# Kernel tuning notes

Hardware: AMD Instinct MI355X
Metric: run time of the kernel (lower is better)

The kernel has to match this reference:

```python
import jax, jax.numpy as jnp
import numpy as np

N_NODES = 100000
N_EDGES = 1600000
DIM = 32
BN_EPS = 1e-5


def setup_inputs() -> dict:
    key = jax.random.key(0)
    ks = jax.random.split(key, 5)
    h = jax.random.normal(ks[0], (N_NODES, DIM), dtype=jnp.float32)
    e = jax.random.normal(ks[1], (N_EDGES, DIM), dtype=jnp.float32)
    norm = jax.random.uniform(ks[2], (N_NODES, 1), dtype=jnp.float32)
    src = jax.random.randint(ks[3], (N_EDGES,), 0, N_NODES, dtype=jnp.int32)
    dst = jax.random.randint(ks[4], (N_EDGES,), 0, N_NODES, dtype=jnp.int32)
    return {
        "h": h, "e": e, "norm": norm, "src": src, "dst": dst,
        "gamma_h": jnp.ones((DIM,), jnp.float32),
        "beta_h": jnp.zeros((DIM,), jnp.float32),
        "gamma_e": jnp.ones((DIM,), jnp.float32),
        "beta_e": jnp.zeros((DIM,), jnp.float32),
    }


def _batch_norm(x, gamma, beta):
    # training-mode BatchNorm1d: biased batch statistics over axis 0
    mean = jnp.mean(x, axis=0)
    var = jnp.var(x, axis=0)
    return (x - mean) * jax.lax.rsqrt(var + BN_EPS) * gamma + beta


def reference(h, e, norm, src, dst, gamma_h, beta_h, gamma_e, beta_e):
    n_nodes = h.shape[0]
    h = h * norm                                  # [N, d]
    # per-edge gate: e_ij = Ce + Dh_src + Eh_dst (all identity projections)
    e_ij = e + h[src] + h[dst]                    # [E, d]
    sigma = jax.nn.sigmoid(e_ij)                  # [E, d]
    # gated weighted-mean aggregation onto destination nodes
    num = jax.ops.segment_sum(sigma * h[src], dst, num_segments=n_nodes)
    den = jax.ops.segment_sum(sigma, dst, num_segments=n_nodes)
    h_new = h + num / (den + 1e-6)                # zero-indegree nodes: h + 0
    h_new = h_new * norm
    # batch norm (training mode), then activation; dropout is identity in eval
    h_out = jax.nn.relu(_batch_norm(h_new, gamma_h, beta_h))
    e_out = jax.nn.relu(_batch_norm(e_ij, gamma_e, beta_e))
    return h_out, e_out
```

## Files before the change

### kernel.cpp

```cpp
#include <hip/hip_runtime.h>

#define NN 100000
#define NE 1600000
#define DIMS 32
static constexpr int SCOPIES = 32;

typedef float fx4 __attribute__((ext_vector_type(4)));

#define NBUCK 1024
#define NPB   98
#define B1    128
#define CHUNK (NE / B1)

static constexpr long long OFF_HNB   = 0;
static constexpr long long OFF_SE    = 1600000;
static constexpr long long OFF_SH    = 1602048;
static constexpr long long OFF_FIN   = 1604096;
static constexpr long long OFF_OFFS  = 1604224;
static constexpr long long OFF_BBASE = 1704226;
static constexpr long long OFF_HIST  = 1705252;
static constexpr long long OFF_REC   = 1836324;
static constexpr long long OFF_EID2  = 5036324;

__device__ __forceinline__ ushort bf16rn(float f) {
  unsigned u = __float_as_uint(f);
  unsigned r = (u + 0x7FFFu + ((u >> 16) & 1u)) >> 16;
  return (ushort)r;
}
__device__ __forceinline__ float bf16tof(ushort s) {
  return __uint_as_float(((unsigned)s) << 16);
}

__global__ __launch_bounds__(256) void k_hn(const float* __restrict__ h,
                                            const float* __restrict__ norm,
                                            ushort* __restrict__ hnb) {
  int i = blockIdx.x * blockDim.x + threadIdx.x;
  if (i >= NN * 8) return;
  float4 v = reinterpret_cast<const float4*>(h)[i];
  float nm = norm[i >> 3];
  ushort4 o;
  o.x = bf16rn(v.x * nm);
  o.y = bf16rn(v.y * nm);
  o.z = bf16rn(v.z * nm);
  o.w = bf16rn(v.w * nm);
  reinterpret_cast<ushort4*>(hnb)[i] = o;
}

__global__ __launch_bounds__(256) void k_bh(const int* __restrict__ dst,
                                            int* __restrict__ hist) {
  __shared__ int cnt[NBUCK];
  const int t = threadIdx.x, b = blockIdx.x;
  for (int j = t; j < NBUCK; j += 256) cnt[j] = 0;
  __syncthreads();
  const int lo = b * CHUNK, hi = lo + CHUNK;
  for (int i = lo + t; i < hi; i += 256) atomicAdd(&cnt[dst[i] / NPB], 1);
  __syncthreads();
  for (int j = t; j < NBUCK; j += 256) hist[j * B1 + b] = cnt[j];
}

__global__ __launch_bounds__(1024) void k_bscan(int* __restrict__ hist,
                                                int* __restrict__ bbase) {
  __shared__ int sh[NBUCK];
  const int t = threadIdx.x;
  int tot = 0;
  for (int i = 0; i < B1; ++i) tot += hist[t * B1 + i];
  sh[t] = tot;
  __syncthreads();
  for (int d = 1; d < NBUCK; d <<= 1) {
    int v = (t >= d) ? sh[t - d] : 0;
    __syncthreads();
    sh[t] += v;
    __syncthreads();
  }
  int excl = sh[t] - tot;
  bbase[t] = excl;
  if (t == NBUCK - 1) bbase[NBUCK] = NE;
  int run = excl;
  for (int i = 0; i < B1; ++i) {
    int c = hist[t * B1 + i];
    hist[t * B1 + i] = run;
    run += c;
  }
}

__global__ __launch_bounds__(256) void k_bscat(const int* __restrict__ src,
                                               const int* __restrict__ dst,
                                               const int* __restrict__ hist,
                                               unsigned long long* __restrict__ rec) {
  __shared__ int cur[NBUCK];
  const int t = threadIdx.x, b = blockIdx.x;
  for (int j = t; j < NBUCK; j += 256) cur[j] = hist[j * B1 + b];
  __syncthreads();
  const int lo = b * CHUNK, hi = lo + CHUNK;
  for (int i = lo + t; i < hi; i += 256) {
    int d = dst[i], s = src[i];
    int bk = d / NPB;
    int pos = atomicAdd(&cur[bk], 1);
    rec[pos] = (unsigned long long)i |
               ((unsigned long long)s << 21) |
               ((unsigned long long)d << 38);
  }
}

__global__ __launch_bounds__(256) void k_bsort(const unsigned long long* __restrict__ rec,
                                               const int* __restrict__ bbase,
                                               int2* __restrict__ eid2,
                                               int* __restrict__ offs) {
  __shared__ int cnt[NPB];
  __shared__ int curq[NPB];
  __shared__ int2 sorted[2048];
  const int t = threadIdx.x, b = blockIdx.x;
  const int base_e = bbase[b];
  const int n = bbase[b + 1] - base_e;
  const int nodebase = b * NPB;
  if (t < NPB) cnt[t] = 0;
  __syncthreads();
  for (int i = t; i < n; i += 256) {
    int d = (int)((rec[base_e + i] >> 38) & 0x1FFFF);
    atomicAdd(&cnt[d - nodebase], 1);
  }
  __syncthreads();
  if (t == 0) {
    int run = 0;
    for (int j = 0; j < NPB; ++j) {
      int c = cnt[j];
      cnt[j] = run;
      curq[j] = run;
      run += c;
    }
  }
  __syncthreads();
  for (int i = t; i < n; i += 256) {
    unsigned long long r = rec[base_e + i];
    int k = (int)(r & 0x1FFFFF);
    int s = (int)((r >> 21) & 0x1FFFF);
    int d = (int)((r >> 38) & 0x1FFFF);
    int pos = atomicAdd(&curq[d - nodebase], 1);
    if (pos < 2048) sorted[pos] = make_int2(k, s);
  }
  __syncthreads();
  for (int i = t; i < n; i += 256) eid2[base_e + i] = sorted[i];
  for (int j = t; j < NPB; j += 256) {
    int node = nodebase + j;
    if (node < NN) offs[node] = base_e + cnt[j];
  }
  if (b == 0 && t == 0) offs[NN] = NE;
}

__global__ __launch_bounds__(256) void k_edge(const float* __restrict__ e,
                                              const ushort* __restrict__ hnb,
                                              const int* __restrict__ src,
                                              const int* __restrict__ dst,
                                              float* __restrict__ stats_e) {
  const int lane = threadIdx.x & 7;
  const int slot0 = (blockIdx.x * blockDim.x + threadIdx.x) >> 3;
  const int S = (gridDim.x * blockDim.x) >> 3;
  float s0 = 0.f, s1 = 0.f, s2 = 0.f, s3 = 0.f;
  float q0 = 0.f, q1 = 0.f, q2 = 0.f, q3 = 0.f;

  const float4*  e4  = reinterpret_cast<const float4*>(e);
  const ushort4* hb4 = reinterpret_cast<const ushort4*>(hnb);

  for (int base = slot0; base < NE; base += 4 * S) {
    const int k0 = base;
    const int k1 = base + S;
    const int k2 = base + 2 * S;
    const int k3 = base + 3 * S;
    const bool v1 = (k1 < NE), v2 = (k2 < NE), v3 = (k3 < NE);
    const int a1 = v1 ? k1 : k0, a2 = v2 ? k2 : k0, a3 = v3 ? k3 : k0;
    const int sc0 = src[k0], dc0 = dst[k0];
    const int sc1 = src[a1], dc1 = dst[a1];
    const int sc2 = src[a2], dc2 = dst[a2];
    const int sc3 = src[a3], dc3 = dst[a3];
    float4  ev0 = e4[(long long)k0 * 8 + lane];
    float4  ev1 = e4[(long long)a1 * 8 + lane];
    float4  ev2 = e4[(long long)a2 * 8 + lane];
    float4  ev3 = e4[(long long)a3 * 8 + lane];
    ushort4 hs0 = hb4[(long long)sc0 * 8 + lane];
    ushort4 hs1 = hb4[(long long)sc1 * 8 + lane];
    ushort4 hs2 = hb4[(long long)sc2 * 8 + lane];
    ushort4 hs3 = hb4[(long long)sc3 * 8 + lane];
    ushort4 hd0 = hb4[(long long)dc0 * 8 + lane];
    ushort4 hd1 = hb4[(long long)dc1 * 8 + lane];
    ushort4 hd2 = hb4[(long long)dc2 * 8 + lane];
    ushort4 hd3 = hb4[(long long)dc3 * 8 + lane];
    {
      float x0 = ev0.x + bf16tof(hs0.x) + bf16tof(hd0.x);
      float x1 = ev0.y + bf16tof(hs0.y) + bf16tof(hd0.y);
      float x2 = ev0.z + bf16tof(hs0.z) + bf16tof(hd0.z);
      float x3 = ev0.w + bf16tof(hs0.w) + bf16tof(hd0.w);
      s0 += x0; s1 += x1; s2 += x2; s3 += x3;
      q0 += x0 * x0; q1 += x1 * x1; q2 += x2 * x2; q3 += x3 * x3;
    }
    if (v1) {
      float x0 = ev1.x + bf16tof(hs1.x) + bf16tof(hd1.x);
      float x1 = ev1.y + bf16tof(hs1.y) + bf16tof(hd1.y);
      float x2 = ev1.z + bf16tof(hs1.z) + bf16tof(hd1.z);
      float x3 = ev1.w + bf16tof(hs1.w) + bf16tof(hd1.w);
      s0 += x0; s1 += x1; s2 += x2; s3 += x3;
      q0 += x0 * x0; q1 += x1 * x1; q2 += x2 * x2; q3 += x3 * x3;
    }
    if (v2) {
      float x0 = ev2.x + bf16tof(hs2.x) + bf16tof(hd2.x);
      float x1 = ev2.y + bf16tof(hs2.y) + bf16tof(hd2.y);
      float x2 = ev2.z + bf16tof(hs2.z) + bf16tof(hd2.z);
      float x3 = ev2.w + bf16tof(hs2.w) + bf16tof(hd2.w);
      s0 += x0; s1 += x1; s2 += x2; s3 += x3;
      q0 += x0 * x0; q1 += x1 * x1; q2 += x2 * x2; q3 += x3 * x3;
    }
    if (v3) {
      float x0 = ev3.x + bf16tof(hs3.x) + bf16tof(hd3.x);
      float x1 = ev3.y + bf16tof(hs3.y) + bf16tof(hd3.y);
      float x2 = ev3.z + bf16tof(hs3.z) + bf16tof(hd3.z);
      float x3 = ev3.w + bf16tof(hs3.w) + bf16tof(hd3.w);
      s0 += x0; s1 += x1; s2 += x2; s3 += x3;
      q0 += x0 * x0; q1 += x1 * x1; q2 += x2 * x2; q3 += x3 * x3;
    }
  }

  __shared__ float sh[64];
  if (threadIdx.x < 64) sh[threadIdx.x] = 0.f;
  __syncthreads();
  const int cb = lane * 4;
  atomicAdd(&sh[cb + 0], s0); atomicAdd(&sh[cb + 1], s1);
  atomicAdd(&sh[cb + 2], s2); atomicAdd(&sh[cb + 3], s3);
  atomicAdd(&sh[32 + cb + 0], q0); atomicAdd(&sh[32 + cb + 1], q1);
  atomicAdd(&sh[32 + cb + 2], q2); atomicAdd(&sh[32 + cb + 3], q3);
  __syncthreads();
  if (threadIdx.x < 64)
    atomicAdd(&stats_e[(blockIdx.x & (SCOPIES - 1)) * 64 + threadIdx.x], sh[threadIdx.x]);
}

__global__ void k_fin_e(const float* __restrict__ stats_e, float* __restrict__ fin) {
  int t = threadIdx.x;
  float s = 0.f, q = 0.f;
  for (int c = 0; c < SCOPIES; ++c) {
    s += stats_e[c * 64 + t];
    q += stats_e[c * 64 + 32 + t];
  }
  float mean = s / (float)NE;
  float var = q / (float)NE - mean * mean;
  fin[64 + t] = mean;
  fin[96 + t] = rsqrtf(var + 1e-5f);
}

__global__ __launch_bounds__(256) void k_agg(const float* __restrict__ e,
                                             const float* __restrict__ h,
                                             const ushort* __restrict__ hnb,
                                             const int* __restrict__ offs,
                                             const int2* __restrict__ eid2,
                                             const float* __restrict__ norm,
                                             const float* __restrict__ fin,
                                             const float* __restrict__ ge,
                                             const float* __restrict__ be,
                                             float* __restrict__ hpre,
                                             float* __restrict__ eout,
                                             float* __restrict__ stats_h) {
  const int g = (blockIdx.x * blockDim.x + threadIdx.x) >> 3;
  const int lane = threadIdx.x & 7;
  const int cb = lane * 4;
  float n0 = 0.f, n1 = 0.f, n2 = 0.f, n3 = 0.f;
  float d0 = 0.f, d1 = 0.f, d2 = 0.f, d3 = 0.f;

  const float4*  e4  = reinterpret_cast<const float4*>(e);
  const ushort4* hb4 = reinterpret_cast<const ushort4*>(hnb);

  float me0 = fin[64 + cb + 0], me1 = fin[64 + cb + 1], me2 = fin[64 + cb + 2], me3 = fin[64 + cb + 3];
  float ie0 = fin[96 + cb + 0], ie1 = fin[96 + cb + 1], ie2 = fin[96 + cb + 2], ie3 = fin[96 + cb + 3];
  float ge0 = ge[cb + 0], ge1 = ge[cb + 1], ge2 = ge[cb + 2], ge3 = ge[cb + 3];
  float be0 = be[cb + 0], be1 = be[cb + 1], be2 = be[cb + 2], be3 = be[cb + 3];

  ushort4 uhv = hb4[(long long)g * 8 + lane];
  float hv0 = bf16tof(uhv.x), hv1 = bf16tof(uhv.y), hv2 = bf16tof(uhv.z), hv3 = bf16tof(uhv.w);
  float nm = norm[g];
  float4 hf = reinterpret_cast<const float4*>(h)[(long long)g * 8 + lane];
  float hw0 = hf.x * nm, hw1 = hf.y * nm, hw2 = hf.z * nm, hw3 = hf.w * nm;

  const int lo = offs[g];
  const int hi = offs[g + 1];

#define AGG_CONSUME(EV, US, KX)                                                   \
  {                                                                               \
    float fs0 = bf16tof(US.x), fs1 = bf16tof(US.y),                               \
          fs2 = bf16tof(US.z), fs3 = bf16tof(US.w);                               \
    float x0 = EV.x + fs0 + hv0;                                                  \
    float x1 = EV.y + fs1 + hv1;                                                  \
    float x2 = EV.z + fs2 + hv2;                                                  \
    float x3 = EV.w + fs3 + hv3;                                                  \
    float g0 = 1.f / (1.f + __expf(-x0));                                         \
    float g1 = 1.f / (1.f + __expf(-x1));                                         \
    float g2 = 1.f / (1.f + __expf(-x2));                                         \
    float g3 = 1.f / (1.f + __expf(-x3));                                         \
    n0 += g0 * fs0; n1 += g1 * fs1; n2 += g2 * fs2; n3 += g3 * fs3;               \
    d0 += g0; d1 += g1; d2 += g2; d3 += g3;                                       \
    fx4 ov;                                                                       \
    ov.x = fmaxf(0.f, (x0 - me0) * ie0 * ge0 + be0);                              \
    ov.y = fmaxf(0.f, (x1 - me1) * ie1 * ge1 + be1);                              \
    ov.z = fmaxf(0.f, (x2 - me2) * ie2 * ge2 + be2);                              \
    ov.w = fmaxf(0.f, (x3 - me3) * ie3 * ge3 + be3);                              \
    __builtin_nontemporal_store(ov, reinterpret_cast<fx4*>(eout) + ((long long)(KX) * 8 + lane)); \
  }

  int p = lo;
  for (; p + 4 <= hi; p += 4) {
    int2 r0 = eid2[p + 0];
    int2 r1 = eid2[p + 1];
    int2 r2 = eid2[p + 2];
    int2 r3 = eid2[p + 3];
    float4  ev0 = e4[(long long)r0.x * 8 + lane];
    float4  ev1 = e4[(long long)r1.x * 8 + lane];
    float4  ev2 = e4[(long long)r2.x * 8 + lane];
    float4  ev3 = e4[(long long)r3.x * 8 + lane];
    ushort4 us0 = hb4[(long long)r0.y * 8 + lane];
    ushort4 us1 = hb4[(long long)r1.y * 8 + lane];
    ushort4 us2 = hb4[(long long)r2.y * 8 + lane];
    ushort4 us3 = hb4[(long long)r3.y * 8 + lane];
    AGG_CONSUME(ev0, us0, r0.x)
    AGG_CONSUME(ev1, us1, r1.x)
    AGG_CONSUME(ev2, us2, r2.x)
    AGG_CONSUME(ev3, us3, r3.x)
  }
  for (; p < hi; ++p) {
    int2 r0 = eid2[p];
    float4  ev0 = e4[(long long)r0.x * 8 + lane];
    ushort4 us0 = hb4[(long long)r0.y * 8 + lane];
    AGG_CONSUME(ev0, us0, r0.x)
  }
#undef AGG_CONSUME

  float y0 = (hw0 + n0 / (d0 + 1e-6f)) * nm;
  float y1 = (hw1 + n1 / (d1 + 1e-6f)) * nm;
  float y2 = (hw2 + n2 / (d2 + 1e-6f)) * nm;
  float y3 = (hw3 + n3 / (d3 + 1e-6f)) * nm;
  reinterpret_cast<float4*>(hpre)[(long long)g * 8 + lane] = make_float4(y0, y1, y2, y3);

  __shared__ float sh[64];
  if (threadIdx.x < 64) sh[threadIdx.x] = 0.f;
  __syncthreads();
  atomicAdd(&sh[cb + 0], y0); atomicAdd(&sh[cb + 1], y1);
  atomicAdd(&sh[cb + 2], y2); atomicAdd(&sh[cb + 3], y3);
  atomicAdd(&sh[32 + cb + 0], y0 * y0); atomicAdd(&sh[32 + cb + 1], y1 * y1);
  atomicAdd(&sh[32 + cb + 2], y2 * y2); atomicAdd(&sh[32 + cb + 3], y3 * y3);
  __syncthreads();
  if (threadIdx.x < 64)
    atomicAdd(&stats_h[(blockIdx.x & (SCOPIES - 1)) * 64 + threadIdx.x], sh[threadIdx.x]);
}

__global__ void k_fin_h(const float* __restrict__ stats_h, float* __restrict__ fin) {
  int t = threadIdx.x;
  float s = 0.f, q = 0.f;
  for (int c = 0; c < SCOPIES; ++c) {
    s += stats_h[c * 64 + t];
    q += stats_h[c * 64 + 32 + t];
  }
  float mean = s / (float)NN;
  float var = q / (float)NN - mean * mean;
  fin[t] = mean;
  fin[32 + t] = rsqrtf(var + 1e-5f);
}

__global__ __launch_bounds__(256) void k_apply(float* __restrict__ buf,
                                               long long nslots,
                                               const float* __restrict__ mean,
                                               const float* __restrict__ inv,
                                               const float* __restrict__ gamma,
                                               const float* __restrict__ beta) {
  long long i = (long long)blockIdx.x * blockDim.x + threadIdx.x;
  if (i >= nslots) return;
  const int cb = (int)(i & 7) * 4;
  float4 x = reinterpret_cast<float4*>(buf)[i];
  float y0 = fmaxf(0.f, (x.x - mean[cb + 0]) * inv[cb + 0] * gamma[cb + 0] + beta[cb + 0]);
  float y1 = fmaxf(0.f, (x.y - mean[cb + 1]) * inv[cb + 1] * gamma[cb + 1] + beta[cb + 1]);
  float y2 = fmaxf(0.f, (x.z - mean[cb + 2]) * inv[cb + 2] * gamma[cb + 2] + beta[cb + 2]);
  float y3 = fmaxf(0.f, (x.w - mean[cb + 3]) * inv[cb + 3] * gamma[cb + 3] + beta[cb + 3]);
  reinterpret_cast<float4*>(buf)[i] = make_float4(y0, y1, y2, y3);
}

extern "C" void kernel_launch(void* const* d_in, const int* in_sizes, int n_in,
                              void* d_out, int out_size, void* d_ws, size_t ws_size,
                              hipStream_t stream) {
  const float* h     = (const float*)d_in[0];
  const float* e     = (const float*)d_in[1];
  const float* norm  = (const float*)d_in[2];
  const int*   src   = (const int*)d_in[3];
  const int*   dst   = (const int*)d_in[4];
  const float* gh    = (const float*)d_in[5];
  const float* bh    = (const float*)d_in[6];
  const float* ge    = (const float*)d_in[7];
  const float* be    = (const float*)d_in[8];
  (void)in_sizes; (void)n_in; (void)out_size; (void)ws_size;

  float*  ws    = (float*)d_ws;
  ushort* hnb   = (ushort*)(ws + OFF_HNB);
  float*  se    = ws + OFF_SE;
  float*  shh   = ws + OFF_SH;
  float*  fin   = ws + OFF_FIN;
  int*    offs  = (int*)(ws + OFF_OFFS);
  int*    bbase = (int*)(ws + OFF_BBASE);
  int*    hist  = (int*)(ws + OFF_HIST);
  unsigned long long* rec = (unsigned long long*)(ws + OFF_REC);
  int2*   eid2  = (int2*)(ws + OFF_EID2);

  float* out  = (float*)d_out;
  float* hpre = out;
  float* eout = out + (long long)NN * DIMS;

  (void)hipMemsetAsync(se, 0, (size_t)(OFF_FIN - OFF_SE) * sizeof(float), stream);

  k_hn<<<(NN * 8 + 255) / 256, 256, 0, stream>>>(h, norm, hnb);
  k_bh<<<B1, 256, 0, stream>>>(dst, hist);
  k_bscan<<<1, NBUCK, 0, stream>>>(hist, bbase);
  k_bscat<<<B1, 256, 0, stream>>>(src, dst, hist, rec);
  k_bsort<<<NBUCK, 256, 0, stream>>>(rec, bbase, eid2, offs);
  k_edge<<<4096, 256, 0, stream>>>(e, hnb, src, dst, se);
  k_fin_e<<<1, 32, 0, stream>>>(se, fin);
  k_agg<<<NN * 8 / 256, 256, 0, stream>>>(e, h, hnb, offs, eid2, norm, fin, ge, be,
                                          hpre, eout, shh);
  k_fin_h<<<1, 32, 0, stream>>>(shh, fin);
  k_apply<<<(NN * 8 + 255) / 256, 256, 0, stream>>>(hpre, (long long)NN * 8,
                                                    fin + 0, fin + 32, gh, bh);
}
```

Baseline: 324.4 us.

## Fuse edge BN statistics into aggregation kernel and normalize edges in a later pass

Removes the separate edge pass that recomputed e_ij to gather batch-norm statistics. The aggregation kernel now accumulates the edge sum and sum of squares, writes raw e_ij, and a later apply kernel normalizes edge outputs in place. One edge read-and-gather pass is traded for an extra read-modify-write of the full edge output buffer. The two finalize kernels are merged into one.

```diff
diff --git a/kernel.cpp b/kernel.cpp
--- a/kernel.cpp
+++ b/kernel.cpp
@@ -147,128 +147,26 @@
   if (b == 0 && t == 0) offs[NN] = NE;
 }
 
-__global__ __launch_bounds__(256) void k_edge(const float* __restrict__ e,
-                                              const ushort* __restrict__ hnb,
-                                              const int* __restrict__ src,
-                                              const int* __restrict__ dst,
-                                              float* __restrict__ stats_e) {
-  const int lane = threadIdx.x & 7;
-  const int slot0 = (blockIdx.x * blockDim.x + threadIdx.x) >> 3;
-  const int S = (gridDim.x * blockDim.x) >> 3;
-  float s0 = 0.f, s1 = 0.f, s2 = 0.f, s3 = 0.f;
-  float q0 = 0.f, q1 = 0.f, q2 = 0.f, q3 = 0.f;
-
-  const float4*  e4  = reinterpret_cast<const float4*>(e);
-  const ushort4* hb4 = reinterpret_cast<const ushort4*>(hnb);
-
-  for (int base = slot0; base < NE; base += 4 * S) {
-    const int k0 = base;
-    const int k1 = base + S;
-    const int k2 = base + 2 * S;
-    const int k3 = base + 3 * S;
-    const bool v1 = (k1 < NE), v2 = (k2 < NE), v3 = (k3 < NE);
-    const int a1 = v1 ? k1 : k0, a2 = v2 ? k2 : k0, a3 = v3 ? k3 : k0;
-    const int sc0 = src[k0], dc0 = dst[k0];
-    const int sc1 = src[a1], dc1 = dst[a1];
-    const int sc2 = src[a2], dc2 = dst[a2];
-    const int sc3 = src[a3], dc3 = dst[a3];
-    float4  ev0 = e4[(long long)k0 * 8 + lane];
-    float4  ev1 = e4[(long long)a1 * 8 + lane];
-    float4  ev2 = e4[(long long)a2 * 8 + lane];
-    float4  ev3 = e4[(long long)a3 * 8 + lane];
-    ushort4 hs0 = hb4[(long long)sc0 * 8 + lane];
-    ushort4 hs1 = hb4[(long long)sc1 * 8 + lane];
-    ushort4 hs2 = hb4[(long long)sc2 * 8 + lane];
-    ushort4 hs3 = hb4[(long long)sc3 * 8 + lane];
-    ushort4 hd0 = hb4[(long long)dc0 * 8 + lane];
-    ushort4 hd1 = hb4[(long long)dc1 * 8 + lane];
-    ushort4 hd2 = hb4[(long long)dc2 * 8 + lane];
-    ushort4 hd3 = hb4[(long long)dc3 * 8 + lane];
-    {
-      float x0 = ev0.x + bf16tof(hs0.x) + bf16tof(hd0.x);
-      float x1 = ev0.y + bf16tof(hs0.y) + bf16tof(hd0.y);
-      float x2 = ev0.z + bf16tof(hs0.z) + bf16tof(hd0.z);
-      float x3 = ev0.w + bf16tof(hs0.w) + bf16tof(hd0.w);
-      s0 += x0; s1 += x1; s2 += x2; s3 += x3;
-      q0 += x0 * x0; q1 += x1 * x1; q2 += x2 * x2; q3 += x3 * x3;
-    }
-    if (v1) {
-      float x0 = ev1.x + bf16tof(hs1.x) + bf16tof(hd1.x);
-      float x1 = ev1.y + bf16tof(hs1.y) + bf16tof(hd1.y);
-      float x2 = ev1.z + bf16tof(hs1.z) + bf16tof(hd1.z);
-      float x3 = ev1.w + bf16tof(hs1.w) + bf16tof(hd1.w);
-      s0 += x0; s1 += x1; s2 += x2; s3 += x3;
-      q0 += x0 * x0; q1 += x1 * x1; q2 += x2 * x2; q3 += x3 * x3;
-    }
-    if (v2) {
-      float x0 = ev2.x + bf16tof(hs2.x) + bf16tof(hd2.x);
-      float x1 = ev2.y + bf16tof(hs2.y) + bf16tof(hd2.y);
-      float x2 = ev2.z + bf16tof(hs2.z) + bf16tof(hd2.z);
-      float x3 = ev2.w + bf16tof(hs2.w) + bf16tof(hd2.w);
-      s0 += x0; s1 += x1; s2 += x2; s3 += x3;
-      q0 += x0 * x0; q1 += x1 * x1; q2 += x2 * x2; q3 += x3 * x3;
-    }
-    if (v3) {
-      float x0 = ev3.x + bf16tof(hs3.x) + bf16tof(hd3.x);
-      float x1 = ev3.y + bf16tof(hs3.y) + bf16tof(hd3.y);
-      float x2 = ev3.z + bf16tof(hs3.z) + bf16tof(hd3.z);
-      float x3 = ev3.w + bf16tof(hs3.w) + bf16tof(hd3.w);
-      s0 += x0; s1 += x1; s2 += x2; s3 += x3;
-      q0 += x0 * x0; q1 += x1 * x1; q2 += x2 * x2; q3 += x3 * x3;
-    }
-  }
-
-  __shared__ float sh[64];
-  if (threadIdx.x < 64) sh[threadIdx.x] = 0.f;
-  __syncthreads();
-  const int cb = lane * 4;
-  atomicAdd(&sh[cb + 0], s0); atomicAdd(&sh[cb + 1], s1);
-  atomicAdd(&sh[cb + 2], s2); atomicAdd(&sh[cb + 3], s3);
-  atomicAdd(&sh[32 + cb + 0], q0); atomicAdd(&sh[32 + cb + 1], q1);
-  atomicAdd(&sh[32 + cb + 2], q2); atomicAdd(&sh[32 + cb + 3], q3);
-  __syncthreads();
-  if (threadIdx.x < 64)
-    atomicAdd(&stats_e[(blockIdx.x & (SCOPIES - 1)) * 64 + threadIdx.x], sh[threadIdx.x]);
-}
-
-__global__ void k_fin_e(const float* __restrict__ stats_e, float* __restrict__ fin) {
-  int t = threadIdx.x;
-  float s = 0.f, q = 0.f;
-  for (int c = 0; c < SCOPIES; ++c) {
-    s += stats_e[c * 64 + t];
-    q += stats_e[c * 64 + 32 + t];
-  }
-  float mean = s / (float)NE;
-  float var = q / (float)NE - mean * mean;
-  fin[64 + t] = mean;
-  fin[96 + t] = rsqrtf(var + 1e-5f);
-}
-
 __global__ __launch_bounds__(256) void k_agg(const float* __restrict__ e,
                                              const float* __restrict__ h,
                                              const ushort* __restrict__ hnb,
                                              const int* __restrict__ offs,
                                              const int2* __restrict__ eid2,
                                              const float* __restrict__ norm,
-                                             const float* __restrict__ fin,
-                                             const float* __restrict__ ge,
-                                             const float* __restrict__ be,
                                              float* __restrict__ hpre,
                                              float* __restrict__ eout,
-                                             float* __restrict__ stats_h) {
+                                             float* __restrict__ stats_h,
+                                             float* __restrict__ stats_e) {
   const int g = (blockIdx.x * blockDim.x + threadIdx.x) >> 3;
   const int lane = threadIdx.x & 7;
   const int cb = lane * 4;
   float n0 = 0.f, n1 = 0.f, n2 = 0.f, n3 = 0.f;
   float d0 = 0.f, d1 = 0.f, d2 = 0.f, d3 = 0.f;
+  float es0 = 0.f, es1 = 0.f, es2 = 0.f, es3 = 0.f;
+  float eq0 = 0.f, eq1 = 0.f, eq2 = 0.f, eq3 = 0.f;
 
   const float4*  e4  = reinterpret_cast<const float4*>(e);
   const ushort4* hb4 = reinterpret_cast<const ushort4*>(hnb);
-
-  float me0 = fin[64 + cb + 0], me1 = fin[64 + cb + 1], me2 = fin[64 + cb + 2], me3 = fin[64 + cb + 3];
-  float ie0 = fin[96 + cb + 0], ie1 = fin[96 + cb + 1], ie2 = fin[96 + cb + 2], ie3 = fin[96 + cb + 3];
-  float ge0 = ge[cb + 0], ge1 = ge[cb + 1], ge2 = ge[cb + 2], ge3 = ge[cb + 3];
-  float be0 = be[cb + 0], be1 = be[cb + 1], be2 = be[cb + 2], be3 = be[cb + 3];
 
   ushort4 uhv = hb4[(long long)g * 8 + lane];
   float hv0 = bf16tof(uhv.x), hv1 = bf16tof(uhv.y), hv2 = bf16tof(uhv.z), hv3 = bf16tof(uhv.w);
@@ -293,11 +191,10 @@
     float g3 = 1.f / (1.f + __expf(-x3));                                         \
     n0 += g0 * fs0; n1 += g1 * fs1; n2 += g2 * fs2; n3 += g3 * fs3;               \
     d0 += g0; d1 += g1; d2 += g2; d3 += g3;                                       \
+    es0 += x0; es1 += x1; es2 += x2; es3 += x3;                                   \
+    eq0 += x0 * x0; eq1 += x1 * x1; eq2 += x2 * x2; eq3 += x3 * x3;               \
     fx4 ov;                                                                       \
-    ov.x = fmaxf(0.f, (x0 - me0) * ie0 * ge0 + be0);                              \
-    ov.y = fmaxf(0.f, (x1 - me1) * ie1 * ge1 + be1);                              \
-    ov.z = fmaxf(0.f, (x2 - me2) * ie2 * ge2 + be2);                              \
-    ov.w = fmaxf(0.f, (x3 - me3) * ie3 * ge3 + be3);                              \
+    ov.x = x0; ov.y = x1; ov.z = x2; ov.w = x3;                                   \
     __builtin_nontemporal_store(ov, reinterpret_cast<fx4*>(eout) + ((long long)(KX) * 8 + lane)); \
   }
 
@@ -334,29 +231,51 @@
   float y3 = (hw3 + n3 / (d3 + 1e-6f)) * nm;
   reinterpret_cast<float4*>(hpre)[(long long)g * 8 + lane] = make_float4(y0, y1, y2, y3);
 
-  __shared__ float sh[64];
-  if (threadIdx.x < 64) sh[threadIdx.x] = 0.f;
-  __syncthreads();
-  atomicAdd(&sh[cb + 0], y0); atomicAdd(&sh[cb + 1], y1);
-  atomicAdd(&sh[cb + 2], y2); atomicAdd(&sh[cb + 3], y3);
-  atomicAdd(&sh[32 + cb + 0], y0 * y0); atomicAdd(&sh[32 + cb + 1], y1 * y1);
-  atomicAdd(&sh[32 + cb + 2], y2 * y2); atomicAdd(&sh[32 + cb + 3], y3 * y3);
-  __syncthreads();
-  if (threadIdx.x < 64)
-    atomicAdd(&stats_h[(blockIdx.x & (SCOPIES - 1)) * 64 + threadIdx.x], sh[threadIdx.x]);
-}
-
-__global__ void k_fin_h(const float* __restrict__ stats_h, float* __restrict__ fin) {
+  __shared__ float sh[128];
+  if (threadIdx.x < 128) sh[threadIdx.x] = 0.f;
+  __syncthreads();
+  atomicAdd(&sh[cb + 0], es0); atomicAdd(&sh[cb + 1], es1);
+  atomicAdd(&sh[cb + 2], es2); atomicAdd(&sh[cb + 3], es3);
+  atomicAdd(&sh[32 + cb + 0], eq0); atomicAdd(&sh[32 + cb + 1], eq1);
+  atomicAdd(&sh[32 + cb + 2], eq2); atomicAdd(&sh[32 + cb + 3], eq3);
+  atomicAdd(&sh[64 + cb + 0], y0); atomicAdd(&sh[64 + cb + 1], y1);
+  atomicAdd(&sh[64 + cb + 2], y2); atomicAdd(&sh[64 + cb + 3], y3);
+  atomicAdd(&sh[96 + cb + 0], y0 * y0); atomicAdd(&sh[96 + cb + 1], y1 * y1);
+  atomicAdd(&sh[96 + cb + 2], y2 * y2); atomicAdd(&sh[96 + cb + 3], y3 * y3);
+  __syncthreads();
+  const int t = threadIdx.x;
+  if (t < 64)
+    atomicAdd(&stats_e[(blockIdx.x & (SCOPIES - 1)) * 64 + t], sh[t]);
+  else if (t < 128)
+    atomicAdd(&stats_h[(blockIdx.x & (SCOPIES - 1)) * 64 + (t - 64)], sh[t]);
+}
+
+__global__ void k_fin(const float* __restrict__ stats_e,
+                      const float* __restrict__ stats_h,
+                      float* __restrict__ fin) {
   int t = threadIdx.x;
-  float s = 0.f, q = 0.f;
-  for (int c = 0; c < SCOPIES; ++c) {
-    s += stats_h[c * 64 + t];
-    q += stats_h[c * 64 + 32 + t];
-  }
-  float mean = s / (float)NN;
-  float var = q / (float)NN - mean * mean;
-  fin[t] = mean;
-  fin[32 + t] = rsqrtf(var + 1e-5f);
+  if (t < 32) {
+    float s = 0.f, q = 0.f;
+    for (int c = 0; c < SCOPIES; ++c) {
+      s += stats_h[c * 64 + t];
+      q += stats_h[c * 64 + 32 + t];
+    }
+    float mean = s / (float)NN;
+    float var = q / (float)NN - mean * mean;
+    fin[t] = mean;
+    fin[32 + t] = rsqrtf(var + 1e-5f);
+  } else {
+    int col = t - 32;
+    float s = 0.f, q = 0.f;
+    for (int c = 0; c < SCOPIES; ++c) {
+      s += stats_e[c * 64 + col];
+      q += stats_e[c * 64 + 32 + col];
+    }
+    float mean = s / (float)NE;
+    float var = q / (float)NE - mean * mean;
+    fin[64 + col] = mean;
+    fin[96 + col] = rsqrtf(var + 1e-5f);
+  }
 }
 
 __global__ __launch_bounds__(256) void k_apply(float* __restrict__ buf,
@@ -412,11 +331,11 @@
   k_bscan<<<1, NBUCK, 0, stream>>>(hist, bbase);
   k_bscat<<<B1, 256, 0, stream>>>(src, dst, hist, rec);
   k_bsort<<<NBUCK, 256, 0, stream>>>(rec, bbase, eid2, offs);
-  k_edge<<<4096, 256, 0, stream>>>(e, hnb, src, dst, se);
-  k_fin_e<<<1, 32, 0, stream>>>(se, fin);
-  k_agg<<<NN * 8 / 256, 256, 0, stream>>>(e, h, hnb, offs, eid2, norm, fin, ge, be,
-                                          hpre, eout, shh);
-  k_fin_h<<<1, 32, 0, stream>>>(shh, fin);
+  k_agg<<<NN * 8 / 256, 256, 0, stream>>>(e, h, hnb, offs, eid2, norm,
+                                          hpre, eout, shh, se);
+  k_fin<<<1, 64, 0, stream>>>(se, shh, fin);
   k_apply<<<(NN * 8 + 255) / 256, 256, 0, stream>>>(hpre, (long long)NN * 8,
                                                     fin + 0, fin + 32, gh, bh);
-}
+  k_apply<<<((long long)NE * 8 + 255) / 256, 256, 0, stream>>>(eout, (long long)NE * 8,
+                                                               fin + 64, fin + 96, ge, be);
+}
```

New measurement: 333.5 us. 1.03x slower.
